# Performance work log

Hardware: AMD Instinct MI355X
Metric: run time of the kernel (lower is better)

The kernel has to match this reference:

```python
import jax, jax.numpy as jnp
import numpy as np

N = 50000      # nodes
E = 800000     # edges (before self-loops)
D_IN = 256     # input feature dim
H = 4          # attention heads
C = 32         # per-head channels
HID = H * C    # 128, concat output dim
BN_EPS = 1e-5


def setup_inputs() -> dict:
    key = jax.random.key(0)
    ks = jax.random.split(key, 24)
    inp = {}
    inp["x"] = jax.random.normal(ks[0], (N, D_IN), jnp.float32)
    inp["edge_index"] = jax.random.randint(ks[1], (2, E), 0, N, jnp.int32)
    # layer 1 GATConv params
    inp["W1"] = jax.random.normal(ks[2], (D_IN, HID), jnp.float32) * (2.0 / (D_IN + HID)) ** 0.5
    inp["att_src1"] = jax.random.normal(ks[3], (H, C), jnp.float32) * 0.1
    inp["att_dst1"] = jax.random.normal(ks[4], (H, C), jnp.float32) * 0.1
    inp["bias1"] = jnp.zeros((HID,), jnp.float32)
    # layer 1 BatchNorm (eval mode)
    inp["gamma1"] = 1.0 + 0.1 * jax.random.normal(ks[5], (HID,), jnp.float32)
    inp["beta1"] = 0.1 * jax.random.normal(ks[6], (HID,), jnp.float32)
    inp["mean1"] = 0.1 * jax.random.normal(ks[7], (HID,), jnp.float32)
    inp["var1"] = 0.5 + jax.random.uniform(ks[8], (HID,), jnp.float32)
    # layer 2 GATConv params
    inp["W2"] = jax.random.normal(ks[9], (HID, HID), jnp.float32) * (2.0 / (HID + HID)) ** 0.5
    inp["att_src2"] = jax.random.normal(ks[10], (H, C), jnp.float32) * 0.1
    inp["att_dst2"] = jax.random.normal(ks[11], (H, C), jnp.float32) * 0.1
    inp["bias2"] = jnp.zeros((HID,), jnp.float32)
    # layer 2 BatchNorm (eval mode)
    inp["gamma2"] = 1.0 + 0.1 * jax.random.normal(ks[12], (HID,), jnp.float32)
    inp["beta2"] = 0.1 * jax.random.normal(ks[13], (HID,), jnp.float32)
    inp["mean2"] = 0.1 * jax.random.normal(ks[14], (HID,), jnp.float32)
    inp["var2"] = 0.5 + jax.random.uniform(ks[15], (HID,), jnp.float32)
    return inp


def _gat_layer(x, src, dst, W, att_src, att_dst, bias):
    # x: [N, D]; src/dst: [Etot] with self-loops already appended
    h = (x @ W).reshape(N, H, C)                       # [N, H, C]
    a_s = jnp.einsum("nhc,hc->nh", h, att_src)         # [N, H]
    a_d = jnp.einsum("nhc,hc->nh", h, att_dst)         # [N, H]
    e = jax.nn.leaky_relu(a_s[src] + a_d[dst], 0.2)    # [Etot, H]
    # edge softmax over incoming edges of each destination node
    m = jax.ops.segment_max(e, dst, num_segments=N)    # [N, H]
    ex = jnp.exp(e - m[dst])                           # [Etot, H]
    den = jax.ops.segment_sum(ex, dst, num_segments=N) # [N, H]
    alpha = ex / (den[dst] + 1e-16)                    # [Etot, H]
    out = jax.ops.segment_sum(h[src] * alpha[:, :, None], dst, num_segments=N)
    return out.reshape(N, HID) + bias                  # concat heads + bias


def _bn_eval(x, gamma, beta, mean, var):
    return (x - mean) * (gamma * jax.lax.rsqrt(var + BN_EPS)) + beta


def reference(x, edge_index, W1, att_src1, att_dst1, bias1, gamma1, beta1, mean1, var1,
              W2, att_src2, att_dst2, bias2, gamma2, beta2, mean2, var2):
    loop = jnp.arange(N, dtype=edge_index.dtype)
    src = jnp.concatenate([edge_index[0], loop])  # PyG GATConv adds self-loops
    dst = jnp.concatenate([edge_index[1], loop])
    h = _gat_layer(x, src, dst, W1, att_src1, att_dst1, bias1)
    h = jax.nn.relu(_bn_eval(h, gamma1, beta1, mean1, var1))  # dropout = identity (eval)
    h = _gat_layer(h, src, dst, W2, att_src2, att_dst2, bias2)
    h = jax.nn.relu(_bn_eval(h, gamma2, beta2, mean2, var2))
    return h
```

## Files before the change

kernel.cpp:

```cpp
#include <hip/hip_runtime.h>
#include <math.h>

#define N_NODES 50000
#define EDGES   800000
#define ETOT    (EDGES + N_NODES)
#define HID     128
#define NH      4

typedef __attribute__((ext_vector_type(8))) short short8;
typedef __attribute__((ext_vector_type(4))) float floatx4;

__device__ inline unsigned short f2bf(float f) {
    unsigned int u = __float_as_uint(f);
    u = u + 0x7FFFu + ((u >> 16) & 1u);
    return (unsigned short)(u >> 16);
}

#define NB 391
#define BCAP 2688
#define CHUNK 4096
#define BIN_BLOCKS ((ETOT + CHUNK - 1) / CHUNK)

__global__ __launch_bounds__(256) void init_cursor_kernel(int* __restrict__ cursor) {
    int t = blockIdx.x * 256 + threadIdx.x;
    if (t < NB) cursor[t] = t * BCAP;
}

__global__ __launch_bounds__(256) void bin_scatter_kernel(const int* __restrict__ ei,
                                                          int* __restrict__ cursor,
                                                          int* __restrict__ binned) {
    __shared__ int histL[NB];
    int t = threadIdx.x;
    for (int b = t; b < NB; b += 256) histL[b] = 0;
    __syncthreads();
    int base = blockIdx.x * CHUNK;
#pragma unroll
    for (int j = 0; j < 16; j++) {
        int e = base + j * 256 + t;
        if (e < ETOT) {
            int d = (e < EDGES) ? ei[EDGES + e] : (e - EDGES);
            atomicAdd(&histL[d >> 7], 1);
        }
    }
    __syncthreads();
    for (int b = t; b < NB; b += 256) {
        int c = histL[b];
        histL[b] = c ? atomicAdd(&cursor[b], c) : 0;
    }
    __syncthreads();
#pragma unroll
    for (int j = 0; j < 16; j++) {
        int e = base + j * 256 + t;
        if (e < ETOT) {
            int s, d;
            if (e < EDGES) { s = ei[e]; d = ei[EDGES + e]; }
            else           { s = d = e - EDGES; }
            int bb = d >> 7;
            int pos = atomicAdd(&histL[bb], 1);
            if (pos < (bb + 1) * BCAP)
                binned[pos] = (s << 7) | (d & 127);
        }
    }
}

__global__ __launch_bounds__(256) void bin_finalize_kernel(const int* __restrict__ binned,
                                                           const int* __restrict__ cursor,
                                                           int* __restrict__ starts,
                                                           int* __restrict__ degs,
                                                           int* __restrict__ csr) {
    __shared__ int histN[128];
    __shared__ int excl[128];
    int b = blockIdx.x, t = threadIdx.x;
    int n0 = b << 7;
    int S = b * BCAP;
    int cnt = cursor[b] - S;
    if (cnt > BCAP) cnt = BCAP;
    if (t < 128) histN[t] = 0;
    __syncthreads();
    for (int j = t; j < cnt; j += 256)
        atomicAdd(&histN[binned[S + j] & 127], 1);
    __syncthreads();
    int v = (t < 128) ? histN[t] : 0;
    if (t < 128) excl[t] = v;
    __syncthreads();
    for (int off = 1; off < 128; off <<= 1) {
        int x = 0, add = 0;
        if (t < 128) { x = excl[t]; if (t >= off) add = excl[t - off]; }
        __syncthreads();
        if (t < 128) excl[t] = x + add;
        __syncthreads();
    }
    if (t < 128) {
        int ex = excl[t] - v;
        int n = n0 + t;
        if (n < N_NODES) { starts[n] = S + ex; degs[n] = v; }
        histN[t] = ex;
    }
    __syncthreads();
    for (int j = t; j < cnt; j += 256) {
        int e = binned[S + j];
        int pos = atomicAdd(&histN[e & 127], 1);
        csr[S + pos] = e >> 7;
    }
}

__global__ void wtrans_coef_kernel(const float* __restrict__ W1, const float* __restrict__ W2,
                                   unsigned short* __restrict__ Wt1, unsigned short* __restrict__ Wt2,
                                   const float* __restrict__ b1, const float* __restrict__ g1,
                                   const float* __restrict__ be1, const float* __restrict__ mn1,
                                   const float* __restrict__ vr1,
                                   const float* __restrict__ b2, const float* __restrict__ g2,
                                   const float* __restrict__ be2, const float* __restrict__ mn2,
                                   const float* __restrict__ vr2, float* __restrict__ coef) {
    int i = blockIdx.x * 256 + threadIdx.x;
    if (i < 256 * 128) { int k = i >> 7, n = i & 127; Wt1[n * 256 + k] = f2bf(W1[i]); }
    if (i < 128 * 128) { int k = i >> 7, n = i & 127; Wt2[n * 128 + k] = f2bf(W2[i]); }
    if (blockIdx.x == 0) {
        int t = threadIdx.x;
        if (t < 128) {
            float sc = g1[t] * rsqrtf(vr1[t] + 1e-5f);
            coef[t]       = sc;
            coef[128 + t] = be1[t] + (b1[t] - mn1[t]) * sc;
        } else {
            int c = t - 128;
            float sc = g2[c] * rsqrtf(vr2[c] + 1e-5f);
            coef[256 + c] = sc;
            coef[384 + c] = be2[c] + (b2[c] - mn2[c]) * sc;
        }
    }
}

#define GR   64
#define KC   64
#define PADK 88
#define PADH 136

union Smem {
    struct { unsigned short Xs[GR][PADK]; unsigned short Ws[HID][PADK]; } s;
    unsigned short Hs[GR][PADH];
};

template<bool XBF16>
__global__ __launch_bounds__(256) void gemm_att_kernel(const void* __restrict__ Xv,
                                                       const unsigned short* __restrict__ Wt,
                                                       const float* __restrict__ att_src,
                                                       const float* __restrict__ att_dst,
                                                       unsigned short* __restrict__ Hout,
                                                       float* __restrict__ aS,
                                                       float* __restrict__ aD, int K) {
    __shared__ Smem sm;
    int t = threadIdx.x, lane = t & 63, w = t >> 6;
    int quad = lane >> 4, nl = lane & 15;
    int rowBase = blockIdx.x * GR;

    floatx4 acc[8];
    floatx4 zero = {0.f, 0.f, 0.f, 0.f};
#pragma unroll
    for (int b = 0; b < 8; b++) acc[b] = zero;

    const float*          Xf = (const float*)Xv;
    const unsigned short* Xb = (const unsigned short*)Xv;

    for (int k0 = 0; k0 < K; k0 += KC) {
#pragma unroll
        for (int it = 0; it < 2; it++) {
            int s5 = t + it * 256;
            int row = s5 >> 3, kg = s5 & 7;
            int gr = rowBase + row;
            unsigned short tmp[8];
            if (XBF16) {
                uint4 v = make_uint4(0, 0, 0, 0);
                if (gr < N_NODES) v = *(const uint4*)&Xb[(unsigned)(gr * K + k0 + kg * 8)];
                *(uint4*)tmp = v;
            } else {
                float4 v0 = make_float4(0, 0, 0, 0), v1 = v0;
                if (gr < N_NODES) {
                    const float* p = &Xf[(unsigned)(gr * K + k0 + kg * 8)];
                    v0 = *(const float4*)p;
                    v1 = *(const float4*)(p + 4);
                }
                tmp[0] = f2bf(v0.x); tmp[1] = f2bf(v0.y); tmp[2] = f2bf(v0.z); tmp[3] = f2bf(v0.w);
                tmp[4] = f2bf(v1.x); tmp[5] = f2bf(v1.y); tmp[6] = f2bf(v1.z); tmp[7] = f2bf(v1.w);
            }
            *(uint4*)&sm.s.Xs[row][kg * 8] = *(uint4*)tmp;
        }
#pragma unroll
        for (int it = 0; it < 4; it++) {
            int s5 = t + it * 256;
            int n = s5 >> 3, kg = s5 & 7;
            *(uint4*)&sm.s.Ws[n][kg * 8] = *(const uint4*)&Wt[(unsigned)(n * K + k0 + kg * 8)];
        }
        __syncthreads();
#pragma unroll
        for (int ks = 0; ks < 2; ks++) {
            int kb = ks * 32 + quad * 8;
            short8 a0 = *(const short8*)&sm.s.Xs[w * 16 + nl][kb];
#pragma unroll
            for (int ct = 0; ct < 8; ct++) {
                short8 b = *(const short8*)&sm.s.Ws[ct * 16 + nl][kb];
                acc[ct] = __builtin_amdgcn_mfma_f32_16x16x32_bf16(a0, b, acc[ct], 0, 0, 0);
            }
        }
        __syncthreads();
    }

#pragma unroll
    for (int ct = 0; ct < 8; ct++)
#pragma unroll
        for (int r = 0; r < 4; r++)
            sm.Hs[w * 16 + quad * 4 + r][ct * 16 + nl] = f2bf(acc[ct][r]);

    float asv[8], adv[8];
    {
        const float* ap = &att_src[nl * 8];
        const float* dp = &att_dst[nl * 8];
        *(float4*)&asv[0] = *(const float4*)ap;  *(float4*)&asv[4] = *(const float4*)(ap + 4);
        *(float4*)&adv[0] = *(const float4*)dp;  *(float4*)&adv[4] = *(const float4*)(dp + 4);
    }
    int hd = nl >> 2;
#pragma unroll
    for (int it = 0; it < 4; it++) {
        int rl = w * 16 + it * 4 + quad;
        int grow = rowBase + rl;
        uint4 v = *(const uint4*)&sm.Hs[rl][nl * 8];
        float f[8];
        f[0] = __uint_as_float(v.x << 16); f[1] = __uint_as_float(v.x & 0xffff0000u);
        f[2] = __uint_as_float(v.y << 16); f[3] = __uint_as_float(v.y & 0xffff0000u);
        f[4] = __uint_as_float(v.z << 16); f[5] = __uint_as_float(v.z & 0xffff0000u);
        f[6] = __uint_as_float(v.w << 16); f[7] = __uint_as_float(v.w & 0xffff0000u);
        float ds = 0.f, dd = 0.f;
#pragma unroll
        for (int j = 0; j < 8; j++) {
            ds = fmaf(f[j], asv[j], ds);
            dd = fmaf(f[j], adv[j], dd);
        }
        ds += __shfl_xor(ds, 1); ds += __shfl_xor(ds, 2);
        dd += __shfl_xor(dd, 1); dd += __shfl_xor(dd, 2);
        if (grow < N_NODES) {
            *(uint4*)&Hout[(unsigned)(grow * HID + nl * 8)] = v;
            if ((nl & 3) == 0) { aS[grow * 4 + hd] = ds; aD[grow * 4 + hd] = dd; }
        }
    }
}

#define ECAP 64
#define ASTRIDE 65

template<bool OUTBF16>
__global__ __launch_bounds__(256) void gather_kernel(const unsigned short* __restrict__ hfeat,
                                                     const float* __restrict__ a_s,
                                                     const float* __restrict__ a_d,
                                                     const int* __restrict__ starts,
                                                     const int* __restrict__ degs,
                                                     const int* __restrict__ csr,
                                                     const float* __restrict__ coefA,
                                                     const float* __restrict__ coefB,
                                                     void* __restrict__ outv) {
    __shared__ float alphaT[4][4][ASTRIDE];
    __shared__ int   offS[4][ECAP];
    int t = threadIdx.x, lane = t & 63, ws = t >> 6;
    int h = lane >> 4, l16 = lane & 15;
    int n = blockIdx.x * 4 + ws;
    int start = starts[n];
    int deg = degs[n];
    float adh = a_d[(unsigned)(n * 4 + h)];

    float e[4];
    int   sreg[4];
#pragma unroll
    for (int it = 0; it < 4; it++) {
        int j = l16 + it * 16;
        e[it] = -1e30f;
        if (j < deg) {
            int s = csr[start + j];
            sreg[it] = s;
            float as = a_s[(unsigned)(s * 4 + h)];
            float v = as + adh;
            e[it] = v > 0.f ? v : 0.2f * v;
        }
    }
    float m = fmaxf(fmaxf(e[0], e[1]), fmaxf(e[2], e[3]));
    for (int j = ECAP + l16; j < deg; j += 16) {
        int s = csr[start + j];
        float as = a_s[(unsigned)(s * 4 + h)];
        float v = as + adh; v = v > 0.f ? v : 0.2f * v;
        m = fmaxf(m, v);
    }
#pragma unroll
    for (int off = 1; off < 16; off <<= 1) m = fmaxf(m, __shfl_xor(m, off));

    float x[4];
    float d = 0.f;
#pragma unroll
    for (int it = 0; it < 4; it++) { x[it] = __expf(e[it] - m); d += x[it]; }
    for (int j = ECAP + l16; j < deg; j += 16) {
        int s = csr[start + j];
        float as = a_s[(unsigned)(s * 4 + h)];
        float v = as + adh; v = v > 0.f ? v : 0.2f * v;
        d += __expf(v - m);
    }
#pragma unroll
    for (int off = 1; off < 16; off <<= 1) d += __shfl_xor(d, off);
    float rd = 1.0f / (d + 1e-16f);

#pragma unroll
    for (int it = 0; it < 4; it++) {
        int j = l16 + it * 16;
        if (j < deg) {
            alphaT[ws][h][j] = x[it] * rd;
            if (h == 0) offS[ws][j] = sreg[it] << 8;
        }
    }
    __syncthreads();

    int c = lane * 2;
    int lane4 = lane * 4;
    const char* hbase = (const char*)hfeat;

    float acc0 = 0.f, acc1 = 0.f;
    int cap = deg < ECAP ? deg : ECAP;
    int j = 0;
    for (; j + 7 < cap; j += 8) {
        unsigned o[8]; float a[8]; unsigned v[8];
#pragma unroll
        for (int u = 0; u < 8; u++) o[u] = (unsigned)(offS[ws][j + u] + lane4);
#pragma unroll
        for (int u = 0; u < 8; u++) a[u] = alphaT[ws][h][j + u];
#pragma unroll
        for (int u = 0; u < 8; u++) v[u] = *(const unsigned int*)(hbase + o[u]);
#pragma unroll
        for (int u = 0; u < 8; u++) {
            acc0 = fmaf(__uint_as_float(v[u] << 16),         a[u], acc0);
            acc1 = fmaf(__uint_as_float(v[u] & 0xffff0000u), a[u], acc1);
        }
    }
    for (; j < cap; j++) {
        unsigned o = (unsigned)(offS[ws][j] + lane4);
        float al = alphaT[ws][h][j];
        unsigned int v = *(const unsigned int*)(hbase + o);
        acc0 = fmaf(__uint_as_float(v << 16),         al, acc0);
        acc1 = fmaf(__uint_as_float(v & 0xffff0000u), al, acc1);
    }
    for (; j < deg; j++) {
        int s = csr[start + j];
        float as = a_s[(unsigned)(s * 4 + h)];
        float v2 = as + adh; v2 = v2 > 0.f ? v2 : 0.2f * v2;
        float al = __expf(v2 - m) * rd;
        unsigned int v = *(const unsigned int*)(hbase + (unsigned)((s << 8) + lane4));
        acc0 = fmaf(__uint_as_float(v << 16),         al, acc0);
        acc1 = fmaf(__uint_as_float(v & 0xffff0000u), al, acc1);
    }
    float2 cA = *(const float2*)&coefA[c];
    float2 cB = *(const float2*)&coefB[c];
    float o0 = fmaxf(fmaf(acc0, cA.x, cB.x), 0.f);
    float o1 = fmaxf(fmaf(acc1, cA.y, cB.y), 0.f);
    if (OUTBF16) {
        unsigned int pk = (unsigned int)f2bf(o0) | ((unsigned int)f2bf(o1) << 16);
        ((unsigned int*)outv)[(unsigned)(n * 64 + lane)] = pk;
    } else {
        ((float2*)outv)[(unsigned)(n * 64 + lane)] = make_float2(o0, o1);
    }
}

extern "C" void kernel_launch(void* const* d_in, const int* in_sizes, int n_in,
                              void* d_out, int out_size, void* d_ws, size_t ws_size,
                              hipStream_t stream) {
    const float* x    = (const float*)d_in[0];
    const int*   ei   = (const int*)d_in[1];
    const float* W1   = (const float*)d_in[2];
    const float* as1  = (const float*)d_in[3];
    const float* ad1  = (const float*)d_in[4];
    const float* b1   = (const float*)d_in[5];
    const float* g1   = (const float*)d_in[6];
    const float* be1  = (const float*)d_in[7];
    const float* mn1  = (const float*)d_in[8];
    const float* vr1  = (const float*)d_in[9];
    const float* W2   = (const float*)d_in[10];
    const float* as2  = (const float*)d_in[11];
    const float* ad2  = (const float*)d_in[12];
    const float* b2   = (const float*)d_in[13];
    const float* g2   = (const float*)d_in[14];
    const float* be2  = (const float*)d_in[15];
    const float* mn2  = (const float*)d_in[16];
    const float* vr2  = (const float*)d_in[17];
    float* out = (float*)d_out;

    unsigned short* hb  = (unsigned short*)d_ws;
    unsigned short* x2b = hb + (size_t)N_NODES * HID;
    unsigned short* Wt1 = x2b + (size_t)N_NODES * HID;
    unsigned short* Wt2 = Wt1 + 128 * 256;
    float* aS    = (float*)(Wt2 + 128 * 128);
    float* aD    = aS + N_NODES * NH;
    float* coef  = aD + N_NODES * NH;
    int* cursor  = (int*)(coef + 512);
    int* starts  = cursor + NB;
    int* degs    = starts + N_NODES;
    int* binned  = degs + N_NODES;
    int* csr     = binned + NB * BCAP;

    init_cursor_kernel<<<2, 256, 0, stream>>>(cursor);
    bin_scatter_kernel<<<BIN_BLOCKS, 256, 0, stream>>>(ei, cursor, binned);
    bin_finalize_kernel<<<NB, 256, 0, stream>>>(binned, cursor, starts, degs, csr);
    wtrans_coef_kernel<<<128, 256, 0, stream>>>(W1, W2, Wt1, Wt2,
                                                b1, g1, be1, mn1, vr1,
                                                b2, g2, be2, mn2, vr2, coef);

    int gemmGrid = (N_NODES + GR - 1) / GR;
    int nodeGrid = N_NODES / 4;

    gemm_att_kernel<false><<<gemmGrid, 256, 0, stream>>>(x, Wt1, as1, ad1, hb, aS, aD, 256);
    gather_kernel<true><<<nodeGrid, 256, 0, stream>>>(hb, aS, aD, starts, degs, csr,
                                                      coef, coef + 128, (void*)x2b);
    gemm_att_kernel<true><<<gemmGrid, 256, 0, stream>>>(x2b, Wt2, as2, ad2, hb, aS, aD, 128);
    gather_kernel<false><<<nodeGrid, 256, 0, stream>>>(hb, aS, aD, starts, degs, csr,
                                                       coef + 256, coef + 384, (void*)out);
}
```

Baseline: 264.7 us.

## Split gather edge loop across two waves per node and fold cursor init into weight kernel

The gather kernel now launches 512 threads per block. Four waves compute the softmax statistics for four nodes, then two waves per node split the neighbor aggregation by interleaving edges, and the partial sums are combined through shared memory. This raises memory-level parallelism for the latency-bound feature gathers, at the cost of an extra barrier, a shared-memory reduction, and half the threads idling during the softmax phase. Separately, the cursor initialization is folded into the weight-transpose kernel to remove one kernel launch.

```diff
diff --git a/kernel.cpp b/kernel.cpp
--- a/kernel.cpp
+++ b/kernel.cpp
@@ -20,11 +20,6 @@
 #define BCAP 2688
 #define CHUNK 4096
 #define BIN_BLOCKS ((ETOT + CHUNK - 1) / CHUNK)
-
-__global__ __launch_bounds__(256) void init_cursor_kernel(int* __restrict__ cursor) {
-    int t = blockIdx.x * 256 + threadIdx.x;
-    if (t < NB) cursor[t] = t * BCAP;
-}
 
 __global__ __launch_bounds__(256) void bin_scatter_kernel(const int* __restrict__ ei,
                                                           int* __restrict__ cursor,
@@ -104,14 +99,15 @@
     }
 }
 
-__global__ void wtrans_coef_kernel(const float* __restrict__ W1, const float* __restrict__ W2,
-                                   unsigned short* __restrict__ Wt1, unsigned short* __restrict__ Wt2,
-                                   const float* __restrict__ b1, const float* __restrict__ g1,
-                                   const float* __restrict__ be1, const float* __restrict__ mn1,
-                                   const float* __restrict__ vr1,
-                                   const float* __restrict__ b2, const float* __restrict__ g2,
-                                   const float* __restrict__ be2, const float* __restrict__ mn2,
-                                   const float* __restrict__ vr2, float* __restrict__ coef) {
+__global__ void wtrans_coef_init_kernel(const float* __restrict__ W1, const float* __restrict__ W2,
+                                        unsigned short* __restrict__ Wt1, unsigned short* __restrict__ Wt2,
+                                        const float* __restrict__ b1, const float* __restrict__ g1,
+                                        const float* __restrict__ be1, const float* __restrict__ mn1,
+                                        const float* __restrict__ vr1,
+                                        const float* __restrict__ b2, const float* __restrict__ g2,
+                                        const float* __restrict__ be2, const float* __restrict__ mn2,
+                                        const float* __restrict__ vr2, float* __restrict__ coef,
+                                        int* __restrict__ cursor) {
     int i = blockIdx.x * 256 + threadIdx.x;
     if (i < 256 * 128) { int k = i >> 7, n = i & 127; Wt1[n * 256 + k] = f2bf(W1[i]); }
     if (i < 128 * 128) { int k = i >> 7, n = i & 127; Wt2[n * 128 + k] = f2bf(W2[i]); }
@@ -127,6 +123,9 @@
             coef[256 + c] = sc;
             coef[384 + c] = be2[c] + (b2[c] - mn2[c]) * sc;
         }
+    }
+    if (blockIdx.x == 1) {
+        for (int b = threadIdx.x; b < NB; b += 256) cursor[b] = b * BCAP;
     }
 }
 
@@ -244,10 +243,10 @@
 }
 
 #define ECAP 64
-#define ASTRIDE 65
+#define ASTRIDE 72
 
 template<bool OUTBF16>
-__global__ __launch_bounds__(256) void gather_kernel(const unsigned short* __restrict__ hfeat,
+__global__ __launch_bounds__(512) void gather_kernel(const unsigned short* __restrict__ hfeat,
                                                      const float* __restrict__ a_s,
                                                      const float* __restrict__ a_d,
                                                      const int* __restrict__ starts,
@@ -258,74 +257,86 @@
                                                      void* __restrict__ outv) {
     __shared__ float alphaT[4][4][ASTRIDE];
     __shared__ int   offS[4][ECAP];
-    int t = threadIdx.x, lane = t & 63, ws = t >> 6;
-    int h = lane >> 4, l16 = lane & 15;
-    int n = blockIdx.x * 4 + ws;
+    __shared__ float accS[4][128];
+    __shared__ float mS[4][4], rdS[4][4];
+    int t = threadIdx.x, lane = t & 63, w = t >> 6;
+    int nodeBase = blockIdx.x * 4;
+
+    if (w < 4) {
+        int n = nodeBase + w;
+        int h = lane >> 4, l16 = lane & 15;
+        int start = starts[n];
+        int deg = degs[n];
+        float adh = a_d[(unsigned)(n * 4 + h)];
+
+        float e[4];
+        int   sreg[4];
+#pragma unroll
+        for (int it = 0; it < 4; it++) {
+            int j = l16 + it * 16;
+            e[it] = -1e30f;
+            if (j < deg) {
+                int s = csr[start + j];
+                sreg[it] = s;
+                float as = a_s[(unsigned)(s * 4 + h)];
+                float v = as + adh;
+                e[it] = v > 0.f ? v : 0.2f * v;
+            }
+        }
+        float m = fmaxf(fmaxf(e[0], e[1]), fmaxf(e[2], e[3]));
+        for (int j = ECAP + l16; j < deg; j += 16) {
+            int s = csr[start + j];
+            float as = a_s[(unsigned)(s * 4 + h)];
+            float v = as + adh; v = v > 0.f ? v : 0.2f * v;
+            m = fmaxf(m, v);
+        }
+#pragma unroll
+        for (int off = 1; off < 16; off <<= 1) m = fmaxf(m, __shfl_xor(m, off));
+
+        float x[4];
+        float d = 0.f;
+#pragma unroll
+        for (int it = 0; it < 4; it++) { x[it] = __expf(e[it] - m); d += x[it]; }
+        for (int j = ECAP + l16; j < deg; j += 16) {
+            int s = csr[start + j];
+            float as = a_s[(unsigned)(s * 4 + h)];
+            float v = as + adh; v = v > 0.f ? v : 0.2f * v;
+            d += __expf(v - m);
+        }
+#pragma unroll
+        for (int off = 1; off < 16; off <<= 1) d += __shfl_xor(d, off);
+        float rd = 1.0f / (d + 1e-16f);
+
+#pragma unroll
+        for (int it = 0; it < 4; it++) {
+            int j = l16 + it * 16;
+            if (j < deg) {
+                alphaT[w][h][j] = x[it] * rd;
+                if (h == 0) offS[w][j] = sreg[it] << 8;
+            }
+        }
+        if (l16 == 0) { mS[w][h] = m; rdS[w][h] = rd; }
+    }
+    __syncthreads();
+
+    int k = w >> 1, p = w & 1;
+    int n = nodeBase + k;
     int start = starts[n];
     int deg = degs[n];
-    float adh = a_d[(unsigned)(n * 4 + h)];
-
-    float e[4];
-    int   sreg[4];
-#pragma unroll
-    for (int it = 0; it < 4; it++) {
-        int j = l16 + it * 16;
-        e[it] = -1e30f;
-        if (j < deg) {
-            int s = csr[start + j];
-            sreg[it] = s;
-            float as = a_s[(unsigned)(s * 4 + h)];
-            float v = as + adh;
-            e[it] = v > 0.f ? v : 0.2f * v;
-        }
-    }
-    float m = fmaxf(fmaxf(e[0], e[1]), fmaxf(e[2], e[3]));
-    for (int j = ECAP + l16; j < deg; j += 16) {
-        int s = csr[start + j];
-        float as = a_s[(unsigned)(s * 4 + h)];
-        float v = as + adh; v = v > 0.f ? v : 0.2f * v;
-        m = fmaxf(m, v);
-    }
-#pragma unroll
-    for (int off = 1; off < 16; off <<= 1) m = fmaxf(m, __shfl_xor(m, off));
-
-    float x[4];
-    float d = 0.f;
-#pragma unroll
-    for (int it = 0; it < 4; it++) { x[it] = __expf(e[it] - m); d += x[it]; }
-    for (int j = ECAP + l16; j < deg; j += 16) {
-        int s = csr[start + j];
-        float as = a_s[(unsigned)(s * 4 + h)];
-        float v = as + adh; v = v > 0.f ? v : 0.2f * v;
-        d += __expf(v - m);
-    }
-#pragma unroll
-    for (int off = 1; off < 16; off <<= 1) d += __shfl_xor(d, off);
-    float rd = 1.0f / (d + 1e-16f);
-
-#pragma unroll
-    for (int it = 0; it < 4; it++) {
-        int j = l16 + it * 16;
-        if (j < deg) {
-            alphaT[ws][h][j] = x[it] * rd;
-            if (h == 0) offS[ws][j] = sreg[it] << 8;
-        }
-    }
-    __syncthreads();
-
     int c = lane * 2;
+    int h = lane >> 4;
     int lane4 = lane * 4;
     const char* hbase = (const char*)hfeat;
 
     float acc0 = 0.f, acc1 = 0.f;
     int cap = deg < ECAP ? deg : ECAP;
-    int j = 0;
-    for (; j + 7 < cap; j += 8) {
+    int j = p;
+    for (; j + 14 < cap; j += 16) {
         unsigned o[8]; float a[8]; unsigned v[8];
 #pragma unroll
-        for (int u = 0; u < 8; u++) o[u] = (unsigned)(offS[ws][j + u] + lane4);
-#pragma unroll
-        for (int u = 0; u < 8; u++) a[u] = alphaT[ws][h][j + u];
+        for (int u = 0; u < 8; u++) o[u] = (unsigned)(offS[k][j + 2 * u] + lane4);
+#pragma unroll
+        for (int u = 0; u < 8; u++) a[u] = alphaT[k][h][j + 2 * u];
 #pragma unroll
         for (int u = 0; u < 8; u++) v[u] = *(const unsigned int*)(hbase + o[u]);
 #pragma unroll
@@ -334,31 +345,42 @@
             acc1 = fmaf(__uint_as_float(v[u] & 0xffff0000u), a[u], acc1);
         }
     }
-    for (; j < cap; j++) {
-        unsigned o = (unsigned)(offS[ws][j] + lane4);
-        float al = alphaT[ws][h][j];
+    for (; j < cap; j += 2) {
+        unsigned o = (unsigned)(offS[k][j] + lane4);
+        float al = alphaT[k][h][j];
         unsigned int v = *(const unsigned int*)(hbase + o);
         acc0 = fmaf(__uint_as_float(v << 16),         al, acc0);
         acc1 = fmaf(__uint_as_float(v & 0xffff0000u), al, acc1);
     }
-    for (; j < deg; j++) {
-        int s = csr[start + j];
-        float as = a_s[(unsigned)(s * 4 + h)];
-        float v2 = as + adh; v2 = v2 > 0.f ? v2 : 0.2f * v2;
-        float al = __expf(v2 - m) * rd;
-        unsigned int v = *(const unsigned int*)(hbase + (unsigned)((s << 8) + lane4));
-        acc0 = fmaf(__uint_as_float(v << 16),         al, acc0);
-        acc1 = fmaf(__uint_as_float(v & 0xffff0000u), al, acc1);
-    }
-    float2 cA = *(const float2*)&coefA[c];
-    float2 cB = *(const float2*)&coefB[c];
-    float o0 = fmaxf(fmaf(acc0, cA.x, cB.x), 0.f);
-    float o1 = fmaxf(fmaf(acc1, cA.y, cB.y), 0.f);
-    if (OUTBF16) {
-        unsigned int pk = (unsigned int)f2bf(o0) | ((unsigned int)f2bf(o1) << 16);
-        ((unsigned int*)outv)[(unsigned)(n * 64 + lane)] = pk;
-    } else {
-        ((float2*)outv)[(unsigned)(n * 64 + lane)] = make_float2(o0, o1);
+    if (deg > ECAP) {
+        float m  = mS[k][h];
+        float rd = rdS[k][h];
+        float adh = a_d[(unsigned)(n * 4 + h)];
+        for (int jj = ECAP + p; jj < deg; jj += 2) {
+            int s = csr[start + jj];
+            float as = a_s[(unsigned)(s * 4 + h)];
+            float v2 = as + adh; v2 = v2 > 0.f ? v2 : 0.2f * v2;
+            float al = __expf(v2 - m) * rd;
+            unsigned int v = *(const unsigned int*)(hbase + (unsigned)((s << 8) + lane4));
+            acc0 = fmaf(__uint_as_float(v << 16),         al, acc0);
+            acc1 = fmaf(__uint_as_float(v & 0xffff0000u), al, acc1);
+        }
+    }
+
+    if (p == 1) *(float2*)&accS[k][c] = make_float2(acc0, acc1);
+    __syncthreads();
+    if (p == 0) {
+        float2 other = *(const float2*)&accS[k][c];
+        float2 cA = *(const float2*)&coefA[c];
+        float2 cB = *(const float2*)&coefB[c];
+        float o0 = fmaxf(fmaf(acc0 + other.x, cA.x, cB.x), 0.f);
+        float o1 = fmaxf(fmaf(acc1 + other.y, cA.y, cB.y), 0.f);
+        if (OUTBF16) {
+            unsigned int pk = (unsigned int)f2bf(o0) | ((unsigned int)f2bf(o1) << 16);
+            ((unsigned int*)outv)[(unsigned)(n * 64 + lane)] = pk;
+        } else {
+            ((float2*)outv)[(unsigned)(n * 64 + lane)] = make_float2(o0, o1);
+        }
     }
 }
 
@@ -398,20 +420,19 @@
     int* binned  = degs + N_NODES;
     int* csr     = binned + NB * BCAP;
 
-    init_cursor_kernel<<<2, 256, 0, stream>>>(cursor);
+    wtrans_coef_init_kernel<<<128, 256, 0, stream>>>(W1, W2, Wt1, Wt2,
+                                                     b1, g1, be1, mn1, vr1,
+                                                     b2, g2, be2, mn2, vr2, coef, cursor);
     bin_scatter_kernel<<<BIN_BLOCKS, 256, 0, stream>>>(ei, cursor, binned);
     bin_finalize_kernel<<<NB, 256, 0, stream>>>(binned, cursor, starts, degs, csr);
-    wtrans_coef_kernel<<<128, 256, 0, stream>>>(W1, W2, Wt1, Wt2,
-                                                b1, g1, be1, mn1, vr1,
-                                                b2, g2, be2, mn2, vr2, coef);
 
     int gemmGrid = (N_NODES + GR - 1) / GR;
     int nodeGrid = N_NODES / 4;
 
     gemm_att_kernel<false><<<gemmGrid, 256, 0, stream>>>(x, Wt1, as1, ad1, hb, aS, aD, 256);
-    gather_kernel<true><<<nodeGrid, 256, 0, stream>>>(hb, aS, aD, starts, degs, csr,
+    gather_kernel<true><<<nodeGrid, 512, 0, stream>>>(hb, aS, aD, starts, degs, csr,
                                                       coef, coef + 128, (void*)x2b);
     gemm_att_kernel<true><<<gemmGrid, 256, 0, stream>>>(x2b, Wt2, as2, ad2, hb, aS, aD, 128);
-    gather_kernel<false><<<nodeGrid, 256, 0, stream>>>(hb, aS, aD, starts, degs, csr,
+    gather_kernel<false><<<nodeGrid, 512, 0, stream>>>(hb, aS, aD, starts, degs, csr,
                                                        coef + 256, coef + 384, (void*)out);
 }
```

Measured after the change: 311.1 us. 17.5% more time.
